# Performance work log

Hardware: AMD Instinct MI355X
Metric: run time of the kernel (lower is better)

Reference implementation:

```python
import jax, jax.numpy as jnp
import numpy as np

B, S = 256, 512
NQ = 1000           # n_skills
MEM, DK, DV, FC = 20, 50, 200, 50  # memory_size, key dim, value dim, final fc dim


def _kaiming(key, shape, fan_in):
    return jax.random.normal(key, shape) * np.float32(np.sqrt(2.0 / fan_in))


def setup_inputs() -> dict:
    key = jax.random.key(0)
    ks = jax.random.split(key, 12)
    q_data = jax.random.randint(ks[0], (B, S), 0, NQ + 1)
    qa_data = jax.random.randint(ks[1], (B, S), 0, 2 * NQ + 1)
    u = jax.random.uniform(ks[2], (B * S,))
    # target: -1 = masked/padding, else binary label (matches target.ge(0) masking)
    target = jnp.where(u < 0.1, -1.0, (u > 0.55).astype(jnp.float32))
    q_embed_w = _kaiming(ks[3], (NQ + 1, DK), DK)
    qa_embed_w = _kaiming(ks[4], (2 * NQ + 1, DV), DV)
    memory_key = _kaiming(ks[5], (MEM, DK), DK)
    init_memory_value = _kaiming(ks[6], (MEM, DV), DV)
    erase_w = _kaiming(ks[7], (DV, DV), DV)
    erase_b = jnp.zeros((DV,), jnp.float32)
    add_w = _kaiming(ks[8], (DV, DV), DV)
    add_b = jnp.zeros((DV,), jnp.float32)
    read_w = _kaiming(ks[9], (DV + FC, FC), DV + FC)
    read_b = jnp.zeros((FC,), jnp.float32)
    pred_w = _kaiming(ks[10], (FC, 1), FC)
    pred_b = jnp.zeros((1,), jnp.float32)
    return dict(q_data=q_data, qa_data=qa_data, target=target,
                q_embed_w=q_embed_w, qa_embed_w=qa_embed_w,
                memory_key=memory_key, init_memory_value=init_memory_value,
                erase_w=erase_w, erase_b=erase_b, add_w=add_w, add_b=add_b,
                read_w=read_w, read_b=read_b, pred_w=pred_w, pred_b=pred_b)


def reference(q_data, qa_data, target, q_embed_w, qa_embed_w, memory_key,
              init_memory_value, erase_w, erase_b, add_w, add_b,
              read_w, read_b, pred_w, pred_b):
    b = q_data.shape[0]
    q_e = q_embed_w[q_data]     # [B,S,DK]
    qa_e = qa_embed_w[qa_data]  # [B,S,DV]
    Mv0 = jnp.broadcast_to(init_memory_value, (b, MEM, DV))

    def step(Mv, xs):
        q_t, qa_t = xs                                        # [B,DK], [B,DV]
        corr = jax.nn.softmax(q_t @ memory_key.T, axis=1)     # [B,MEM] addressing
        read = jnp.einsum('bm,bmd->bd', corr, Mv)             # weighted read
        erase = jax.nn.sigmoid(qa_t @ erase_w + erase_b)      # [B,DV]
        add = jnp.tanh(qa_t @ add_w + add_b)                  # [B,DV]
        w = corr[:, :, None]                                  # [B,MEM,1]
        Mv = Mv * (1.0 - w * erase[:, None, :]) + w * add[:, None, :]
        return Mv, read

    _, reads = jax.lax.scan(step, Mv0, (q_e.transpose(1, 0, 2), qa_e.transpose(1, 0, 2)))
    reads = reads.transpose(1, 0, 2)                          # [B,S,DV]
    x = jnp.concatenate([reads, q_e], axis=-1)                # [B,S,DV+FC]
    h = jnp.tanh(x @ read_w + read_b)                         # [B,S,FC]
    logits = (h @ pred_w + pred_b).reshape(-1)                # [B*S]
    mask = target >= 0.0
    t = jnp.where(mask, target, 0.0)
    # numerically-stable BCE-with-logits, masked mean
    bce = jnp.maximum(logits, 0.0) - logits * t + jnp.log1p(jnp.exp(-jnp.abs(logits)))
    loss = jnp.sum(jnp.where(mask, bce, 0.0)) / jnp.maximum(mask.sum(), 1)
    return loss, jax.nn.sigmoid(logits)
```

## Files before the change

### kernel.cpp

```cpp
#include <hip/hip_runtime.h>
#include <math.h>

#define B_   256
#define S_   512
#define NQ_  1000
#define MEM_ 20
#define DK_  50
#define DV_  200
#define FC_  50
#define RPB  4
#define CHK  16
#define CLEN (S_/CHK)
#define NKS  7
#define XS_STRIDE 232
#define NB_EA    ((2*NQ_+1+RPB-1)/RPB)
#define NB_CORR  4
#define NB_WPACK 7
#define NB_HQ    251
#define PREP1_BLOCKS (NB_EA+NB_CORR)
#define MM_BLOCKS (B_*CHK)
#define SCANA_BLOCKS (B_*(CHK-1))
#define SCANA_TOTAL (SCANA_BLOCKS+NB_WPACK+NB_HQ)

typedef __attribute__((ext_vector_type(8))) short bf16x8_t;
typedef __attribute__((ext_vector_type(4))) float f32x4_t;
typedef __attribute__((ext_vector_type(2))) float f32x2_t;

static __device__ __forceinline__ f32x2_t pkfma(f32x2_t a, f32x2_t b, f32x2_t c){
  return __builtin_elementwise_fma(a, b, c);
}

static __device__ __forceinline__ unsigned short f2bf(float f){
  unsigned u = __float_as_uint(f);
  unsigned r = u + 0x7fffu + ((u >> 16) & 1u);
  return (unsigned short)(r >> 16);
}
static __device__ __forceinline__ float bf2f_lo(unsigned v){ return __uint_as_float(v << 16); }
static __device__ __forceinline__ float bf2f_hi(unsigned v){ return __uint_as_float(v & 0xffff0000u); }
static __device__ __forceinline__ float ftanh(float x){
  float e = __expf(2.f*x);
  return 1.f - 2.f*__builtin_amdgcn_rcpf(e+1.f);
}
static __device__ __forceinline__ float fsigm(float x){
  return __builtin_amdgcn_rcpf(1.f+__expf(-x));
}

__global__ __launch_bounds__(256) void k_prep1(
    const float* __restrict__ qaw,
    const float* __restrict__ ew, const float* __restrict__ eb,
    const float* __restrict__ aw, const float* __restrict__ ab,
    float2* __restrict__ eaTab,
    const float* __restrict__ qw, const float* __restrict__ mk,
    float* __restrict__ corrTab){
  __shared__ float qa[RPB*DV_];
  int blk = blockIdx.x;
  if(blk < NB_EA){
    int row0 = blk*RPB;
    for(int i=threadIdx.x; i<RPB*DV_; i+=256){
      int r = i/DV_, cc = i - r*DV_;
      int row = row0 + r;
      qa[i] = (row <= 2*NQ_) ? qaw[row*DV_+cc] : 0.f;
    }
    __syncthreads();
    int d = threadIdx.x;
    if(d >= DV_) return;
    float accE[RPB], accA[RPB];
    #pragma unroll
    for(int r=0;r<RPB;++r){ accE[r] = eb[d]; accA[r] = ab[d]; }
    float we0 = ew[d], wa0 = aw[d];
    for(int j=0;j<DV_;++j){
      int jn = (j+1 < DV_) ? j+1 : j;
      float we1 = ew[jn*DV_+d];
      float wa1 = aw[jn*DV_+d];
      #pragma unroll
      for(int r=0;r<RPB;++r){
        float x = qa[r*DV_+j];
        accE[r] = fmaf(x, we0, accE[r]);
        accA[r] = fmaf(x, wa0, accA[r]);
      }
      we0 = we1; wa0 = wa1;
    }
    #pragma unroll
    for(int r=0;r<RPB;++r){
      int row = row0 + r;
      if(row <= 2*NQ_)
        eaTab[(size_t)row*DV_+d] = make_float2(fsigm(accE[r]), ftanh(accA[r]));
    }
  } else {
    int q = (blk-NB_EA)*256 + threadIdx.x;
    if(q > NQ_) return;
    float qv[DK_];
    #pragma unroll
    for(int j=0;j<DK_;++j) qv[j] = qw[q*DK_+j];
    float s[MEM_]; float mx = -1e30f;
    #pragma unroll
    for(int m=0;m<MEM_;++m){
      float acc = 0.f;
      #pragma unroll
      for(int j=0;j<DK_;++j) acc = fmaf(qv[j], mk[m*DK_+j], acc);
      s[m] = acc; mx = fmaxf(mx, acc);
    }
    float sum = 0.f;
    #pragma unroll
    for(int m=0;m<MEM_;++m){ s[m] = __expf(s[m]-mx); sum += s[m]; }
    float inv = __builtin_amdgcn_rcpf(sum);
    #pragma unroll
    for(int m=0;m<MEM_;++m) corrTab[q*MEM_+m] = s[m]*inv;
  }
}

__global__ __launch_bounds__(256,8) void k_scanA(const int* __restrict__ qd,
    const int* __restrict__ qad,
    const float4* __restrict__ corr4,
    const float2* __restrict__ eaTab,
    unsigned* __restrict__ ABu,
    const float* __restrict__ qw,
    const float* __restrict__ rw, const float* __restrict__ rb,
    const float* __restrict__ pw,
    unsigned short* __restrict__ WpFrag, float* __restrict__ pwPad,
    float* __restrict__ hq){
  const int blk = blockIdx.x;
  if(blk >= SCANA_BLOCKS){
    int xblk = blk - SCANA_BLOCKS;
    if(xblk < NB_WPACK){
      int ks = xblk;
      int nt = threadIdx.x >> 6;
      int lane = threadIdx.x & 63;
      int quad = lane >> 4, col = lane & 15;
      int n = nt*16 + col;
      unsigned short tmp[8];
      #pragma unroll
      for(int j=0;j<8;++j){
        int k = ks*32 + quad*8 + j;
        tmp[j] = (k < DV_ && n < FC_) ? f2bf(rw[k*FC_+n]) : (unsigned short)0;
      }
      uint4* dst = reinterpret_cast<uint4*>(WpFrag + ((size_t)(ks*4+nt)*64 + lane)*8);
      *dst = *reinterpret_cast<const uint4*>(tmp);
      if(ks == 0 && threadIdx.x < 64)
        pwPad[threadIdx.x] = (threadIdx.x < FC_) ? pw[threadIdx.x] : 0.f;
    } else {
      int idx = (xblk-NB_WPACK)*256 + threadIdx.x;
      int q = idx >> 6, n = idx & 63;
      if(q > NQ_) return;
      float v = 0.f;
      if(n < FC_){
        float acc = rb[n];
        #pragma unroll
        for(int j=0;j<DK_;++j)
          acc = fmaf(qw[q*DK_+j], rw[(DV_+j)*FC_+n], acc);
        v = acc;
      }
      hq[q*64+n] = v;
    }
    return;
  }

  const int b = blk / (CHK-1), c = blk % (CHK-1);
  const int d = threadIdx.x;
  const int dc = (d < DV_) ? d : DV_-1;
  const bool act = (d < DV_);
  const int* __restrict__ qp  = qd  + b*S_ + c*CLEN;
  const int* __restrict__ qap = qad + b*S_ + c*CLEN;

  f32x2_t A2[MEM_/2], B2[MEM_/2];
  #pragma unroll
  for(int i=0;i<MEM_/2;++i){ A2[i] = (f32x2_t){1.f,1.f}; B2[i] = (f32x2_t){0.f,0.f}; }

  int q2   = qp[1];
  int qaT2 = qap[2];
  int qaT3 = qap[3];
  int q1s  = __builtin_amdgcn_readfirstlane(qp[0]);
  const float4* cb0 = corr4 + q1s*5;
  float4 c0 = cb0[0], c1 = cb0[1], c2 = cb0[2], c3 = cb0[3], c4 = cb0[4];
  float2 ea  = eaTab[(size_t)qap[0]*DV_ + dc];
  float2 ean = eaTab[(size_t)qap[1]*DV_ + dc];

  #pragma unroll 2
  for(int t=0;t<CLEN;++t){
    int t2 = (t+2 < CLEN) ? t+2 : CLEN-1;
    int t4 = (t+4 < CLEN) ? t+4 : CLEN-1;
    int q3 = qp[t2];
    int qaN = qap[t4];
    int qs = __builtin_amdgcn_readfirstlane(q2);
    const float4* cb = corr4 + qs*5;
    float4 n0 = cb[0], n1 = cb[1], n2 = cb[2], n3 = cb[3], n4 = cb[4];
    float2 eann = eaTab[(size_t)qaT2*DV_ + dc];

    const f32x2_t e2 = {ea.x, ea.x}, a2 = {ea.y, ea.y}, one2 = {1.f, 1.f};
    #define UPDA(cx, cy, i) { \
      f32x2_t cp = {cx, cy}; \
      f32x2_t al = pkfma(-cp, e2, one2); \
      f32x2_t be = cp*a2; \
      A2[i] = A2[i]*al; \
      B2[i] = pkfma(al, B2[i], be); }
    UPDA(c0.x, c0.y, 0)  UPDA(c0.z, c0.w, 1)
    UPDA(c1.x, c1.y, 2)  UPDA(c1.z, c1.w, 3)
    UPDA(c2.x, c2.y, 4)  UPDA(c2.z, c2.w, 5)
    UPDA(c3.x, c3.y, 6)  UPDA(c3.z, c3.w, 7)
    UPDA(c4.x, c4.y, 8)  UPDA(c4.z, c4.w, 9)
    #undef UPDA

    c0=n0; c1=n1; c2=n2; c3=n3; c4=n4;
    ea=ean; ean=eann;
    q2=q3; qaT2=qaT3; qaT3=qaN;
  }
  if(act){
    unsigned* base = ABu + ((size_t)(b*(CHK-1) + c)*MEM_)*DV_ + d;
    #pragma unroll
    for(int i=0;i<MEM_/2;++i){
      base[(size_t)(2*i)*DV_]   = (unsigned)f2bf(A2[i][0]) | ((unsigned)f2bf(B2[i][0]) << 16);
      base[(size_t)(2*i+1)*DV_] = (unsigned)f2bf(A2[i][1]) | ((unsigned)f2bf(B2[i][1]) << 16);
    }
  }
}

__global__ __launch_bounds__(256) void k_prefix(const float* __restrict__ mv0,
    const unsigned* __restrict__ ABu, unsigned short* __restrict__ Mv0s){
  int i = blockIdx.x*256 + threadIdx.x;
  if(i >= B_*MEM_*DV_) return;
  int d = i % DV_;
  int m = (i / DV_) % MEM_;
  int b = i / (DV_*MEM_);
  unsigned abv[CHK-1];
  #pragma unroll
  for(int c=0;c<CHK-1;++c)
    abv[c] = ABu[((size_t)(b*(CHK-1) + c)*MEM_ + m)*DV_ + d];
  float Mv = mv0[m*DV_+d];
  #pragma unroll
  for(int c=1;c<CHK;++c){
    unsigned v = abv[c-1];
    Mv = fmaf(bf2f_lo(v), Mv, bf2f_hi(v));
    Mv0s[((size_t)(b*CHK + c)*MEM_ + m)*DV_ + d] = f2bf(Mv);
  }
}

__global__ __launch_bounds__(256,8) void k_scan_mm(const int* __restrict__ qd,
    const int* __restrict__ qad,
    const float4* __restrict__ corr4,
    const float2* __restrict__ eaTab,
    const float* __restrict__ mv0,
    const unsigned short* __restrict__ Mv0s,
    const unsigned short* __restrict__ WpFrag,
    const float* __restrict__ hq,
    const float* __restrict__ pwPad, const float* __restrict__ pb,
    const float* __restrict__ target,
    float* __restrict__ out, float2* __restrict__ partials){
  __shared__ unsigned short Xs[CLEN*XS_STRIDE];
  __shared__ float sred[2][2][16];
  __shared__ float sbce[4];

  const int blk = blockIdx.x;
  const int b = blk >> 4, c = blk & (CHK-1);
  const int d = threadIdx.x;
  const int dc = (d < DV_) ? d : DV_-1;
  const bool act = (d < DV_);
  const bool padw = (d < 224);
  const int* __restrict__ qp  = qd  + b*S_ + c*CLEN;
  const int* __restrict__ qap = qad + b*S_ + c*CLEN;

  const int wave = threadIdx.x >> 6;
  const int lane = threadIdx.x & 63;
  const int col  = lane & 15, quad = lane >> 4;
  const int rt   = wave & 1;
  const int nh   = wave >> 1;
  const int mbase = rt*16;

  int qpre[4];
  #pragma unroll
  for(int reg=0;reg<4;++reg) qpre[reg] = qp[mbase + quad*4 + reg];

  f32x2_t Mv2[MEM_/2];
  if(c == 0){
    #pragma unroll
    for(int i=0;i<MEM_/2;++i)
      Mv2[i] = (f32x2_t){ mv0[(2*i)*DV_+dc], mv0[(2*i+1)*DV_+dc] };
  } else {
    const unsigned short* base = Mv0s + ((size_t)(b*CHK + c)*MEM_)*DV_ + dc;
    #pragma unroll
    for(int i=0;i<MEM_/2;++i)
      Mv2[i] = (f32x2_t){ bf2f_lo((unsigned)base[(size_t)(2*i)*DV_]),
                          bf2f_lo((unsigned)base[(size_t)(2*i+1)*DV_]) };
  }

  int q2   = qp[1];
  int qaT2 = qap[2];
  int qaT3 = qap[3];
  int q1s  = __builtin_amdgcn_readfirstlane(qp[0]);
  const float4* cbi = corr4 + q1s*5;
  float4 c0 = cbi[0], c1 = cbi[1], c2 = cbi[2], c3 = cbi[3], c4 = cbi[4];
  float2 ea  = eaTab[(size_t)qap[0]*DV_ + dc];
  float2 ean = eaTab[(size_t)qap[1]*DV_ + dc];

  #pragma unroll 2
  for(int t=0;t<CLEN;++t){
    int t2 = (t+2 < CLEN) ? t+2 : CLEN-1;
    int t4 = (t+4 < CLEN) ? t+4 : CLEN-1;
    int q3 = qp[t2];
    int qaN = qap[t4];
    int qs = __builtin_amdgcn_readfirstlane(q2);
    const float4* cb = corr4 + qs*5;
    float4 n0 = cb[0], n1 = cb[1], n2 = cb[2], n3 = cb[3], n4 = cb[4];
    float2 eann = eaTab[(size_t)qaT2*DV_ + dc];

    const f32x2_t e2 = {ea.x, ea.x}, a2 = {ea.y, ea.y};
    f32x2_t rd2 = {0.f, 0.f};
    #define UPD2(cx, cy, i) { \
      f32x2_t cp = {cx, cy}; \
      rd2 = pkfma(cp, Mv2[i], rd2); \
      Mv2[i] = pkfma(cp, pkfma(-Mv2[i], e2, a2), Mv2[i]); }
    UPD2(c0.x, c0.y, 0)  UPD2(c0.z, c0.w, 1)
    UPD2(c1.x, c1.y, 2)  UPD2(c1.z, c1.w, 3)
    UPD2(c2.x, c2.y, 4)  UPD2(c2.z, c2.w, 5)
    UPD2(c3.x, c3.y, 6)  UPD2(c3.z, c3.w, 7)
    UPD2(c4.x, c4.y, 8)  UPD2(c4.z, c4.w, 9)
    #undef UPD2

    if(padw) Xs[t*XS_STRIDE + d] = act ? f2bf(rd2[0]+rd2[1]) : (unsigned short)0;

    c0=n0; c1=n1; c2=n2; c3=n3; c4=n4;
    ea=ean; ean=eann;
    q2=q3; qaT2=qaT3; qaT3=qaN;
  }
  __syncthreads();

  float hqv[4][2];
  #pragma unroll
  for(int reg=0;reg<4;++reg)
    #pragma unroll
    for(int j=0;j<2;++j)
      hqv[reg][j] = hq[qpre[reg]*64 + (nh*2+j)*16 + col];

  f32x4_t acc[2];
  acc[0] = (f32x4_t){0.f,0.f,0.f,0.f};
  acc[1] = (f32x4_t){0.f,0.f,0.f,0.f};

  #pragma unroll
  for(int ks=0;ks<NKS;++ks){
    bf16x8_t a = *reinterpret_cast<const bf16x8_t*>(Xs + (mbase+col)*XS_STRIDE + quad*8 + ks*32);
    #pragma unroll
    for(int j=0;j<2;++j){
      int nt = nh*2 + j;
      bf16x8_t bfr = *reinterpret_cast<const bf16x8_t*>(WpFrag + ((size_t)(ks*4+nt)*64 + lane)*8);
      acc[j] = __builtin_amdgcn_mfma_f32_16x16x32_bf16(a, bfr, acc[j], 0, 0, 0);
    }
  }

  float part[4];
  #pragma unroll
  for(int reg=0;reg<4;++reg){
    float s = 0.f;
    #pragma unroll
    for(int j=0;j<2;++j){
      int n = (nh*2+j)*16 + col;
      float h = acc[j][reg] + hqv[reg][j];
      s = fmaf(pwPad[n], ftanh(h), s);
    }
    part[reg] = s;
  }
  #pragma unroll
  for(int off=1; off<16; off<<=1){
    #pragma unroll
    for(int reg=0;reg<4;++reg) part[reg] += __shfl_xor(part[reg], off, 64);
  }
  if(col == 0){
    #pragma unroll
    for(int reg=0;reg<4;++reg) sred[rt][nh][quad*4+reg] = part[reg];
  }
  __syncthreads();

  float bce = 0.f, cnt = 0.f;
  if(nh == 0 && col == 0){
    float pbv = pb[0];
    #pragma unroll
    for(int reg=0;reg<4;++reg){
      int idx = quad*4 + reg;
      int mloc = mbase + idx;
      int row = b*S_ + c*CLEN + mloc;
      float logit = sred[rt][0][idx] + sred[rt][1][idx] + pbv;
      out[1+row] = fsigm(logit);
      float t = target[row];
      if(t >= 0.f){
        cnt += 1.f;
        bce += fmaxf(logit,0.f) - logit*t + log1pf(__expf(-fabsf(logit)));
      }
    }
  }
  bce += __shfl_xor(bce, 16, 64); cnt += __shfl_xor(cnt, 16, 64);
  bce += __shfl_xor(bce, 32, 64); cnt += __shfl_xor(cnt, 32, 64);
  if(lane == 0 && nh == 0){ sbce[wave] = bce; sbce[2+wave] = cnt; }
  __syncthreads();
  if(threadIdx.x == 0)
    partials[blk] = make_float2(sbce[0]+sbce[1], sbce[2]+sbce[3]);
}

__global__ __launch_bounds__(256) void k_fin(const float2* __restrict__ partials,
                                             float* __restrict__ out){
  float bce = 0.f, cnt = 0.f;
  for(int i=threadIdx.x; i<MM_BLOCKS; i+=256){
    float2 p = partials[i];
    bce += p.x; cnt += p.y;
  }
  #pragma unroll
  for(int off=32; off>0; off>>=1){
    bce += __shfl_down(bce, off, 64);
    cnt += __shfl_down(cnt, off, 64);
  }
  __shared__ float sb[4], sc[4];
  int w = threadIdx.x >> 6;
  if((threadIdx.x & 63) == 0){ sb[w] = bce; sc[w] = cnt; }
  __syncthreads();
  if(threadIdx.x == 0){
    float Bt = sb[0]+sb[1]+sb[2]+sb[3];
    float Ct = sc[0]+sc[1]+sc[2]+sc[3];
    out[0] = Bt / fmaxf(Ct, 1.f);
  }
}

extern "C" void kernel_launch(void* const* d_in, const int* in_sizes, int n_in,
                              void* d_out, int out_size, void* d_ws, size_t ws_size,
                              hipStream_t stream){
  const int*   qd     = (const int*)d_in[0];
  const int*   qad    = (const int*)d_in[1];
  const float* target = (const float*)d_in[2];
  const float* qw     = (const float*)d_in[3];
  const float* qaw    = (const float*)d_in[4];
  const float* mk     = (const float*)d_in[5];
  const float* mv0    = (const float*)d_in[6];
  const float* ew     = (const float*)d_in[7];
  const float* eb     = (const float*)d_in[8];
  const float* aw     = (const float*)d_in[9];
  const float* ab     = (const float*)d_in[10];
  const float* rw     = (const float*)d_in[11];
  const float* rb     = (const float*)d_in[12];
  const float* pw     = (const float*)d_in[13];
  const float* pb     = (const float*)d_in[14];
  float* out = (float*)d_out;

  char* ws = (char*)d_ws;
  size_t off = 0;
  float2* partials = (float2*)(ws + off);            off += (size_t)MM_BLOCKS*8;
  float* corrTab  = (float*)(ws + off);              off += (((size_t)(NQ_+1)*MEM_*4 + 255)/256)*256;
  float2* eaTab   = (float2*)(ws + off);             off += (((size_t)(2*NQ_+1)*DV_*8 + 255)/256)*256;
  unsigned* ABu   = (unsigned*)(ws + off);           off += (size_t)SCANA_BLOCKS*MEM_*DV_*4;
  unsigned short* Mv0s = (unsigned short*)(ws + off); off += (size_t)MM_BLOCKS*MEM_*DV_*2;
  unsigned short* WpFrag = (unsigned short*)(ws + off); off += ((size_t)NKS*4*64*8*2 + 255)/256*256;
  float* pwPad    = (float*)(ws + off);              off += 256;
  float* hq       = (float*)(ws + off);              off += (size_t)(NQ_+1)*64*4;

  k_prep1<<<dim3(PREP1_BLOCKS), dim3(256), 0, stream>>>(qaw, ew, eb, aw, ab, eaTab,
                                                        qw, mk, corrTab);
  k_scanA<<<dim3(SCANA_TOTAL), dim3(256), 0, stream>>>(qd, qad, (const float4*)corrTab, (const float2*)eaTab,
                                                       ABu, qw, rw, rb, pw, WpFrag, pwPad, hq);
  k_prefix<<<dim3((B_*MEM_*DV_+255)/256), dim3(256), 0, stream>>>(mv0, ABu, Mv0s);
  k_scan_mm<<<dim3(MM_BLOCKS), dim3(256), 0, stream>>>(qd, qad, (const float4*)corrTab, (const float2*)eaTab,
                                                       mv0, Mv0s, WpFrag, hq, pwPad, pb, target, out, partials);
  k_fin<<<dim3(1), dim3(256), 0, stream>>>(partials, out);
}
```

Measured before the change: 228.1 us.

## Switch memory scan recurrences and tables to packed fp16 arithmetic

Converts the chunked memory-value scan in both scan kernels from packed fp32 to packed fp16 math (v_pk_fma_f16, fdot2 for the weighted read). The correlation and erase/add tables are stored as fp16, with the erase/add values pre-splatted so they can be used directly as half2 operands. The prefix kernel now handles memory slot pairs and writes packed half2 state. This halves register and ALU width for the serial recurrence and cuts table bandwidth, at the cost of fp16 precision and range over 32-step chunk products.

```diff
diff --git a/kernel.cpp b/kernel.cpp
--- a/kernel.cpp
+++ b/kernel.cpp
@@ -13,6 +13,7 @@
 #define CLEN (S_/CHK)
 #define NKS  7
 #define XS_STRIDE 232
+#define CORR_STRIDE 12
 #define NB_EA    ((2*NQ_+1+RPB-1)/RPB)
 #define NB_CORR  4
 #define NB_WPACK 7
@@ -24,9 +25,16 @@
 
 typedef __attribute__((ext_vector_type(8))) short bf16x8_t;
 typedef __attribute__((ext_vector_type(4))) float f32x4_t;
-typedef __attribute__((ext_vector_type(2))) float f32x2_t;
-
-static __device__ __forceinline__ f32x2_t pkfma(f32x2_t a, f32x2_t b, f32x2_t c){
+typedef __attribute__((ext_vector_type(2))) _Float16 f16x2_t;
+
+static __device__ __forceinline__ f16x2_t h2(unsigned u){ return __builtin_bit_cast(f16x2_t, u); }
+static __device__ __forceinline__ unsigned h2u(f16x2_t v){ return __builtin_bit_cast(unsigned, v); }
+static __device__ __forceinline__ unsigned packh2(float x, float y){
+  unsigned short bx = __builtin_bit_cast(unsigned short, (_Float16)x);
+  unsigned short by = __builtin_bit_cast(unsigned short, (_Float16)y);
+  return (unsigned)bx | ((unsigned)by << 16);
+}
+static __device__ __forceinline__ f16x2_t pkfma16(f16x2_t a, f16x2_t b, f16x2_t c){
   return __builtin_elementwise_fma(a, b, c);
 }
 
@@ -36,7 +44,6 @@
   return (unsigned short)(r >> 16);
 }
 static __device__ __forceinline__ float bf2f_lo(unsigned v){ return __uint_as_float(v << 16); }
-static __device__ __forceinline__ float bf2f_hi(unsigned v){ return __uint_as_float(v & 0xffff0000u); }
 static __device__ __forceinline__ float ftanh(float x){
   float e = __expf(2.f*x);
   return 1.f - 2.f*__builtin_amdgcn_rcpf(e+1.f);
@@ -49,9 +56,9 @@
     const float* __restrict__ qaw,
     const float* __restrict__ ew, const float* __restrict__ eb,
     const float* __restrict__ aw, const float* __restrict__ ab,
-    float2* __restrict__ eaTab,
+    uint2* __restrict__ eaTab,
     const float* __restrict__ qw, const float* __restrict__ mk,
-    float* __restrict__ corrTab){
+    unsigned* __restrict__ corrH){
   __shared__ float qa[RPB*DV_];
   int blk = blockIdx.x;
   if(blk < NB_EA){
@@ -83,8 +90,11 @@
     #pragma unroll
     for(int r=0;r<RPB;++r){
       int row = row0 + r;
-      if(row <= 2*NQ_)
-        eaTab[(size_t)row*DV_+d] = make_float2(fsigm(accE[r]), ftanh(accA[r]));
+      if(row <= 2*NQ_){
+        unsigned he = (unsigned)__builtin_bit_cast(unsigned short, (_Float16)fsigm(accE[r]));
+        unsigned ha = (unsigned)__builtin_bit_cast(unsigned short, (_Float16)ftanh(accA[r]));
+        eaTab[(size_t)row*DV_+d] = make_uint2(he*0x10001u, ha*0x10001u);
+      }
     }
   } else {
     int q = (blk-NB_EA)*256 + threadIdx.x;
@@ -105,14 +115,15 @@
     for(int m=0;m<MEM_;++m){ s[m] = __expf(s[m]-mx); sum += s[m]; }
     float inv = __builtin_amdgcn_rcpf(sum);
     #pragma unroll
-    for(int m=0;m<MEM_;++m) corrTab[q*MEM_+m] = s[m]*inv;
+    for(int i=0;i<MEM_/2;++i)
+      corrH[q*CORR_STRIDE+i] = packh2(s[2*i]*inv, s[2*i+1]*inv);
   }
 }
 
 __global__ __launch_bounds__(256,8) void k_scanA(const int* __restrict__ qd,
     const int* __restrict__ qad,
-    const float4* __restrict__ corr4,
-    const float2* __restrict__ eaTab,
+    const unsigned* __restrict__ corrH,
+    const uint2* __restrict__ eaTab,
     unsigned* __restrict__ ABu,
     const float* __restrict__ qw,
     const float* __restrict__ rw, const float* __restrict__ rb,
@@ -162,18 +173,21 @@
   const int* __restrict__ qp  = qd  + b*S_ + c*CLEN;
   const int* __restrict__ qap = qad + b*S_ + c*CLEN;
 
-  f32x2_t A2[MEM_/2], B2[MEM_/2];
-  #pragma unroll
-  for(int i=0;i<MEM_/2;++i){ A2[i] = (f32x2_t){1.f,1.f}; B2[i] = (f32x2_t){0.f,0.f}; }
+  const f16x2_t one2h = {(_Float16)1.f, (_Float16)1.f};
+  f16x2_t A2[MEM_/2], B2[MEM_/2];
+  #pragma unroll
+  for(int i=0;i<MEM_/2;++i){ A2[i] = one2h; B2[i] = (f16x2_t){(_Float16)0.f,(_Float16)0.f}; }
 
   int q2   = qp[1];
   int qaT2 = qap[2];
   int qaT3 = qap[3];
   int q1s  = __builtin_amdgcn_readfirstlane(qp[0]);
-  const float4* cb0 = corr4 + q1s*5;
-  float4 c0 = cb0[0], c1 = cb0[1], c2 = cb0[2], c3 = cb0[3], c4 = cb0[4];
-  float2 ea  = eaTab[(size_t)qap[0]*DV_ + dc];
-  float2 ean = eaTab[(size_t)qap[1]*DV_ + dc];
+  const unsigned* cp0 = corrH + q1s*CORR_STRIDE;
+  uint4 ca = *(const uint4*)(cp0);
+  uint4 cb = *(const uint4*)(cp0+4);
+  uint2 cc = *(const uint2*)(cp0+8);
+  uint2 ea  = eaTab[(size_t)qap[0]*DV_ + dc];
+  uint2 ean = eaTab[(size_t)qap[1]*DV_ + dc];
 
   #pragma unroll 2
   for(int t=0;t<CLEN;++t){
@@ -182,25 +196,25 @@
     int q3 = qp[t2];
     int qaN = qap[t4];
     int qs = __builtin_amdgcn_readfirstlane(q2);
-    const float4* cb = corr4 + qs*5;
-    float4 n0 = cb[0], n1 = cb[1], n2 = cb[2], n3 = cb[3], n4 = cb[4];
-    float2 eann = eaTab[(size_t)qaT2*DV_ + dc];
-
-    const f32x2_t e2 = {ea.x, ea.x}, a2 = {ea.y, ea.y}, one2 = {1.f, 1.f};
-    #define UPDA(cx, cy, i) { \
-      f32x2_t cp = {cx, cy}; \
-      f32x2_t al = pkfma(-cp, e2, one2); \
-      f32x2_t be = cp*a2; \
+    const float* cpn_ = (const float*)(corrH + qs*CORR_STRIDE);
+    uint4 na = *(const uint4*)(cpn_);
+    uint4 nb = *(const uint4*)(cpn_+4);
+    uint2 nc = *(const uint2*)(cpn_+8);
+    uint2 eann = eaTab[(size_t)qaT2*DV_ + dc];
+
+    const f16x2_t ee = h2(ea.x), aa = h2(ea.y);
+    #define UPDA(u, i) { \
+      f16x2_t cp = h2(u); \
+      f16x2_t al = pkfma16(-cp, ee, one2h); \
+      f16x2_t be = cp*aa; \
       A2[i] = A2[i]*al; \
-      B2[i] = pkfma(al, B2[i], be); }
-    UPDA(c0.x, c0.y, 0)  UPDA(c0.z, c0.w, 1)
-    UPDA(c1.x, c1.y, 2)  UPDA(c1.z, c1.w, 3)
-    UPDA(c2.x, c2.y, 4)  UPDA(c2.z, c2.w, 5)
-    UPDA(c3.x, c3.y, 6)  UPDA(c3.z, c3.w, 7)
-    UPDA(c4.x, c4.y, 8)  UPDA(c4.z, c4.w, 9)
+      B2[i] = pkfma16(al, B2[i], be); }
+    UPDA(ca.x, 0)  UPDA(ca.y, 1)  UPDA(ca.z, 2)  UPDA(ca.w, 3)
+    UPDA(cb.x, 4)  UPDA(cb.y, 5)  UPDA(cb.z, 6)  UPDA(cb.w, 7)
+    UPDA(cc.x, 8)  UPDA(cc.y, 9)
     #undef UPDA
 
-    c0=n0; c1=n1; c2=n2; c3=n3; c4=n4;
+    ca=na; cb=nb; cc=nc;
     ea=ean; ean=eann;
     q2=q3; qaT2=qaT3; qaT3=qaN;
   }
@@ -208,38 +222,39 @@
     unsigned* base = ABu + ((size_t)(b*(CHK-1) + c)*MEM_)*DV_ + d;
     #pragma unroll
     for(int i=0;i<MEM_/2;++i){
-      base[(size_t)(2*i)*DV_]   = (unsigned)f2bf(A2[i][0]) | ((unsigned)f2bf(B2[i][0]) << 16);
-      base[(size_t)(2*i+1)*DV_] = (unsigned)f2bf(A2[i][1]) | ((unsigned)f2bf(B2[i][1]) << 16);
+      unsigned a01 = h2u(A2[i]);
+      unsigned b01 = h2u(B2[i]);
+      base[(size_t)(2*i)*DV_]   = (a01 & 0xffffu) | (b01 << 16);
+      base[(size_t)(2*i+1)*DV_] = (a01 >> 16)     | (b01 & 0xffff0000u);
     }
   }
 }
 
 __global__ __launch_bounds__(256) void k_prefix(const float* __restrict__ mv0,
-    const unsigned* __restrict__ ABu, unsigned short* __restrict__ Mv0s){
+    const unsigned* __restrict__ ABu, unsigned* __restrict__ Mv0p){
   int i = blockIdx.x*256 + threadIdx.x;
-  if(i >= B_*MEM_*DV_) return;
+  if(i >= B_*(MEM_/2)*DV_) return;
   int d = i % DV_;
-  int m = (i / DV_) % MEM_;
-  int b = i / (DV_*MEM_);
-  unsigned abv[CHK-1];
-  #pragma unroll
-  for(int c=0;c<CHK-1;++c)
-    abv[c] = ABu[((size_t)(b*(CHK-1) + c)*MEM_ + m)*DV_ + d];
-  float Mv = mv0[m*DV_+d];
+  int p = (i / DV_) % (MEM_/2);
+  int b = i / (DV_*(MEM_/2));
+  float MvE = mv0[(2*p)*DV_+d];
+  float MvO = mv0[(2*p+1)*DV_+d];
   #pragma unroll
   for(int c=1;c<CHK;++c){
-    unsigned v = abv[c-1];
-    Mv = fmaf(bf2f_lo(v), Mv, bf2f_hi(v));
-    Mv0s[((size_t)(b*CHK + c)*MEM_ + m)*DV_ + d] = f2bf(Mv);
+    unsigned vE = ABu[((size_t)(b*(CHK-1) + (c-1))*MEM_ + 2*p)*DV_ + d];
+    unsigned vO = ABu[((size_t)(b*(CHK-1) + (c-1))*MEM_ + 2*p+1)*DV_ + d];
+    MvE = fmaf((float)h2(vE)[0], MvE, (float)h2(vE)[1]);
+    MvO = fmaf((float)h2(vO)[0], MvO, (float)h2(vO)[1]);
+    Mv0p[((size_t)(b*CHK + c)*(MEM_/2) + p)*DV_ + d] = packh2(MvE, MvO);
   }
 }
 
 __global__ __launch_bounds__(256,8) void k_scan_mm(const int* __restrict__ qd,
     const int* __restrict__ qad,
-    const float4* __restrict__ corr4,
-    const float2* __restrict__ eaTab,
+    const unsigned* __restrict__ corrH,
+    const uint2* __restrict__ eaTab,
     const float* __restrict__ mv0,
-    const unsigned short* __restrict__ Mv0s,
+    const unsigned* __restrict__ Mv0p,
     const unsigned short* __restrict__ WpFrag,
     const float* __restrict__ hq,
     const float* __restrict__ pwPad, const float* __restrict__ pb,
@@ -269,27 +284,28 @@
   #pragma unroll
   for(int reg=0;reg<4;++reg) qpre[reg] = qp[mbase + quad*4 + reg];
 
-  f32x2_t Mv2[MEM_/2];
+  f16x2_t Mv2[MEM_/2];
   if(c == 0){
     #pragma unroll
     for(int i=0;i<MEM_/2;++i)
-      Mv2[i] = (f32x2_t){ mv0[(2*i)*DV_+dc], mv0[(2*i+1)*DV_+dc] };
+      Mv2[i] = (f16x2_t){ (_Float16)mv0[(2*i)*DV_+dc], (_Float16)mv0[(2*i+1)*DV_+dc] };
   } else {
-    const unsigned short* base = Mv0s + ((size_t)(b*CHK + c)*MEM_)*DV_ + dc;
+    const unsigned* base = Mv0p + ((size_t)(b*CHK + c)*(MEM_/2))*DV_ + dc;
     #pragma unroll
     for(int i=0;i<MEM_/2;++i)
-      Mv2[i] = (f32x2_t){ bf2f_lo((unsigned)base[(size_t)(2*i)*DV_]),
-                          bf2f_lo((unsigned)base[(size_t)(2*i+1)*DV_]) };
+      Mv2[i] = h2(base[(size_t)i*DV_]);
   }
 
   int q2   = qp[1];
   int qaT2 = qap[2];
   int qaT3 = qap[3];
   int q1s  = __builtin_amdgcn_readfirstlane(qp[0]);
-  const float4* cbi = corr4 + q1s*5;
-  float4 c0 = cbi[0], c1 = cbi[1], c2 = cbi[2], c3 = cbi[3], c4 = cbi[4];
-  float2 ea  = eaTab[(size_t)qap[0]*DV_ + dc];
-  float2 ean = eaTab[(size_t)qap[1]*DV_ + dc];
+  const unsigned* cp0 = corrH + q1s*CORR_STRIDE;
+  uint4 ca = *(const uint4*)(cp0);
+  uint4 cb = *(const uint4*)(cp0+4);
+  uint2 cc = *(const uint2*)(cp0+8);
+  uint2 ea  = eaTab[(size_t)qap[0]*DV_ + dc];
+  uint2 ean = eaTab[(size_t)qap[1]*DV_ + dc];
 
   #pragma unroll 2
   for(int t=0;t<CLEN;++t){
@@ -298,26 +314,27 @@
     int q3 = qp[t2];
     int qaN = qap[t4];
     int qs = __builtin_amdgcn_readfirstlane(q2);
-    const float4* cb = corr4 + qs*5;
-    float4 n0 = cb[0], n1 = cb[1], n2 = cb[2], n3 = cb[3], n4 = cb[4];
-    float2 eann = eaTab[(size_t)qaT2*DV_ + dc];
-
-    const f32x2_t e2 = {ea.x, ea.x}, a2 = {ea.y, ea.y};
-    f32x2_t rd2 = {0.f, 0.f};
-    #define UPD2(cx, cy, i) { \
-      f32x2_t cp = {cx, cy}; \
-      rd2 = pkfma(cp, Mv2[i], rd2); \
-      Mv2[i] = pkfma(cp, pkfma(-Mv2[i], e2, a2), Mv2[i]); }
-    UPD2(c0.x, c0.y, 0)  UPD2(c0.z, c0.w, 1)
-    UPD2(c1.x, c1.y, 2)  UPD2(c1.z, c1.w, 3)
-    UPD2(c2.x, c2.y, 4)  UPD2(c2.z, c2.w, 5)
-    UPD2(c3.x, c3.y, 6)  UPD2(c3.z, c3.w, 7)
-    UPD2(c4.x, c4.y, 8)  UPD2(c4.z, c4.w, 9)
+    const unsigned* cpn_ = corrH + qs*CORR_STRIDE;
+    uint4 na = *(const uint4*)(cpn_);
+    uint4 nb = *(const uint4*)(cpn_+4);
+    uint2 nc = *(const uint2*)(cpn_+8);
+    uint2 eann = eaTab[(size_t)qaT2*DV_ + dc];
+
+    const f16x2_t ee = h2(ea.x), aa = h2(ea.y);
+    float rd0 = 0.f, rd1 = 0.f;
+    #define UPD2(u, i, acc) { \
+      f16x2_t cp = h2(u); \
+      acc = __builtin_amdgcn_fdot2(cp, Mv2[i], acc, false); \
+      f16x2_t tt = pkfma16(-Mv2[i], ee, aa); \
+      Mv2[i] = pkfma16(cp, tt, Mv2[i]); }
+    UPD2(ca.x, 0, rd0)  UPD2(ca.y, 1, rd1)  UPD2(ca.z, 2, rd0)  UPD2(ca.w, 3, rd1)
+    UPD2(cb.x, 4, rd0)  UPD2(cb.y, 5, rd1)  UPD2(cb.z, 6, rd0)  UPD2(cb.w, 7, rd1)
+    UPD2(cc.x, 8, rd0)  UPD2(cc.y, 9, rd1)
     #undef UPD2
 
-    if(padw) Xs[t*XS_STRIDE + d] = act ? f2bf(rd2[0]+rd2[1]) : (unsigned short)0;
-
-    c0=n0; c1=n1; c2=n2; c3=n3; c4=n4;
+    if(padw) Xs[t*XS_STRIDE + d] = act ? f2bf(rd0+rd1) : (unsigned short)0;
+
+    ca=na; cb=nb; cc=nc;
     ea=ean; ean=eann;
     q2=q3; qaT2=qaT3; qaT3=qaN;
   }
@@ -439,20 +456,20 @@
   char* ws = (char*)d_ws;
   size_t off = 0;
   float2* partials = (float2*)(ws + off);            off += (size_t)MM_BLOCKS*8;
-  float* corrTab  = (float*)(ws + off);              off += (((size_t)(NQ_+1)*MEM_*4 + 255)/256)*256;
-  float2* eaTab   = (float2*)(ws + off);             off += (((size_t)(2*NQ_+1)*DV_*8 + 255)/256)*256;
+  unsigned* corrH = (unsigned*)(ws + off);           off += (((size_t)(NQ_+1)*CORR_STRIDE*4 + 255)/256)*256;
+  uint2* eaTab    = (uint2*)(ws + off);              off += (((size_t)(2*NQ_+1)*DV_*8 + 255)/256)*256;
   unsigned* ABu   = (unsigned*)(ws + off);           off += (size_t)SCANA_BLOCKS*MEM_*DV_*4;
-  unsigned short* Mv0s = (unsigned short*)(ws + off); off += (size_t)MM_BLOCKS*MEM_*DV_*2;
+  unsigned* Mv0p  = (unsigned*)(ws + off);           off += (size_t)MM_BLOCKS*(MEM_/2)*DV_*4;
   unsigned short* WpFrag = (unsigned short*)(ws + off); off += ((size_t)NKS*4*64*8*2 + 255)/256*256;
   float* pwPad    = (float*)(ws + off);              off += 256;
   float* hq       = (float*)(ws + off);              off += (size_t)(NQ_+1)*64*4;
 
   k_prep1<<<dim3(PREP1_BLOCKS), dim3(256), 0, stream>>>(qaw, ew, eb, aw, ab, eaTab,
-                                                        qw, mk, corrTab);
-  k_scanA<<<dim3(SCANA_TOTAL), dim3(256), 0, stream>>>(qd, qad, (const float4*)corrTab, (const float2*)eaTab,
+                                                        qw, mk, corrH);
+  k_scanA<<<dim3(SCANA_TOTAL), dim3(256), 0, stream>>>(qd, qad, corrH, eaTab,
                                                        ABu, qw, rw, rb, pw, WpFrag, pwPad, hq);
-  k_prefix<<<dim3((B_*MEM_*DV_+255)/256), dim3(256), 0, stream>>>(mv0, ABu, Mv0s);
-  k_scan_mm<<<dim3(MM_BLOCKS), dim3(256), 0, stream>>>(qd, qad, (const float4*)corrTab, (const float2*)eaTab,
-                                                       mv0, Mv0s, WpFrag, hq, pwPad, pb, target, out, partials);
+  k_prefix<<<dim3((B_*(MEM_/2)*DV_+255)/256), dim3(256), 0, stream>>>(mv0, ABu, Mv0p);
+  k_scan_mm<<<dim3(MM_BLOCKS), dim3(256), 0, stream>>>(qd, qad, corrH, eaTab,
+                                                       mv0, Mv0p, WpFrag, hq, pwPad, pb, target, out, partials);
   k_fin<<<dim3(1), dim3(256), 0, stream>>>(partials, out);
 }
```

New measurement: 224.4 us. No clear change (-1.6%).
